# Kernel optimization log

Hardware: AMD Instinct MI355X
Metric: run time of the kernel (lower is better)

## Reference

```python
import jax, jax.numpy as jnp
import numpy as np

B, N, K, C_IN, D = 4, 2048, 16, 480, 64
EPS = 1e-5


def _c1(x, w, b):
    # 1x1 Conv1d: x (B,C,N), w (O,C) -> (B,O,N)
    return jnp.einsum('oc,bcn->bon', w, x) + b[:, None]


def _c2(x, w, b):
    # 1x1 Conv2d: x (B,C,J,N), w (O,C) -> (B,O,J,N)
    return jnp.einsum('oc,bcjn->bojn', w, x) + b[:, None, None]


def _bn(x, g, b):
    # eval-mode BatchNorm2d with running_mean=0, running_var=1
    return x * (g / jnp.sqrt(1.0 + EPS))[:, None, None] + b[:, None, None]


def _mlp_res(x, w1, b1, w2, b2, ws, bs):
    return _c1(jax.nn.relu(_c1(x, w1, b1)), w2, b2) + _c1(x, ws, bs)


def _group(f, idx):
    # f (B,C,N), idx (B,K,N) int -> out[b,c,j,n] = f[b,c,idx[b,j,n]]  -> (B,C,K,N)
    return jax.vmap(lambda ff, ii: ff[:, ii])(f, idx)


def _knn_idx(xyz):
    # xyz (B,3,N) -> idx (B,K,N), excluding the self point (nearest neighbor)
    pts = xyz.transpose(0, 2, 1)  # (B,N,3)
    sq = jnp.sum(pts * pts, -1)
    d2 = sq[:, :, None] + sq[:, None, :] - 2.0 * jnp.einsum('bnd,bmd->bnm', pts, pts)
    _, idx = jax.lax.top_k(-d2, K + 1)  # (B,N,K+1), nearest first
    return idx.transpose(0, 2, 1)[:, 1:, :]  # drop self -> (B,K,N)


def _forward(idx, feature, xyz, bt1_w, bt1_b, bt2_w, bt2_b, bts_w, bts_b,
             q_w, q_b, k_w, k_b, v_w, v_b,
             fd1_w, fd1_b, fd_g, fd_bb, fd2_w, fd2_b,
             fg1_w, fg1_b, fg_g, fg_bb, fg2_w, fg2_b,
             at_w, at_b, m41_w, m41_b, m42_w, m42_b):
    x = _mlp_res(feature, bt1_w, bt1_b, bt2_w, bt2_b, bts_w, bts_b)  # (B,64,N)
    q = _c1(x, q_w, q_b)
    k = _c1(x, k_w, k_b)
    v = _c1(x, v_w, v_b)

    group_xyz = _group(xyz, idx)                       # (B,3,K,N)
    rel_xyz = xyz[:, :, None, :] - group_xyz           # (B,3,K,N)
    pos_enc = _c2(jax.nn.relu(_bn(_c2(rel_xyz, fd1_w, fd1_b), fd_g, fd_bb)), fd2_w, fd2_b)  # (B,64,K,N)

    k_local = _group(k, idx)                           # (B,64,K,N)
    v_local = _group(v, idx)
    qk_rel = q[:, :, None, :] - k_local
    attn = _c2(jax.nn.relu(_bn(_c2(qk_rel + pos_enc, fg1_w, fg1_b), fg_g, fg_bb)), fg2_w, fg2_b)  # (B,64,K,N)

    attn1 = attn.transpose(0, 1, 3, 2)                 # (B,64,N,K)
    # ConvTranspose2d(64,64,(4,1),(4,1)) with kernel==stride: out[b,o,4n+r,f] = sum_c x[b,c,n,f]*W[c,o,r] + bias[o]
    y = jnp.einsum('bcnf,cor->bonrf', attn1, at_w)
    y = y.reshape(y.shape[0], y.shape[1], -1, y.shape[4]) + at_b[None, :, None, None]  # (B,64,4N,K)
    attn = jax.nn.softmax(y, axis=1)

    value_rel = (v_local + pos_enc).transpose(0, 1, 3, 2)   # (B,64,N,K)
    value = jnp.repeat(value_rel, 4, axis=2)                # nearest upsample (4,1) -> (B,64,4N,K)

    res = jnp.einsum('bmnf,bmnf->bmn', attn, value)         # (B,64,4N)
    identity = jnp.repeat(x, 4, axis=2)                     # nearest upsample x4 -> (B,64,4N)
    res = res + identity
    completion = _c1(jax.nn.relu(_c1(res, m41_w, m41_b)), m42_w, m42_b)  # (B,3,4N)
    return completion, res


def setup_inputs() -> dict:
    key = jax.random.key(0)
    ks = jax.random.split(key, 24)
    i = iter(range(24))

    def w(shape):
        return (jax.random.normal(ks[next(i)], shape, dtype=jnp.float32) * 0.05)

    z = lambda n: jnp.zeros((n,), jnp.float32)
    o = lambda n: jnp.ones((n,), jnp.float32)
    return {
        'feature': jax.random.normal(ks[next(i)], (B, C_IN, N), dtype=jnp.float32),
        'xyz': jax.random.normal(ks[next(i)], (B, 3, N), dtype=jnp.float32),
        'bt1_w': w((D, C_IN)), 'bt1_b': z(D),
        'bt2_w': w((D, D)), 'bt2_b': z(D),
        'bts_w': w((D, C_IN)), 'bts_b': z(D),
        'q_w': w((D, D)), 'q_b': z(D),
        'k_w': w((D, D)), 'k_b': z(D),
        'v_w': w((D, D)), 'v_b': z(D),
        'fd1_w': w((D, 3)), 'fd1_b': z(D), 'fd_g': o(D), 'fd_bb': z(D),
        'fd2_w': w((D, D)), 'fd2_b': z(D),
        'fg1_w': w((4 * D, D)), 'fg1_b': z(4 * D), 'fg_g': o(4 * D), 'fg_bb': z(4 * D),
        'fg2_w': w((D, 4 * D)), 'fg2_b': z(D),
        'at_w': w((D, D, 4)), 'at_b': z(D),
        'm41_w': w((D, D)), 'm41_b': z(D),
        'm42_w': w((3, D)), 'm42_b': z(3),
    }


def reference(feature, xyz, bt1_w, bt1_b, bt2_w, bt2_b, bts_w, bts_b,
              q_w, q_b, k_w, k_b, v_w, v_b,
              fd1_w, fd1_b, fd_g, fd_bb, fd2_w, fd2_b,
              fg1_w, fg1_b, fg_g, fg_bb, fg2_w, fg2_b,
              at_w, at_b, m41_w, m41_b, m42_w, m42_b):
    idx = _knn_idx(xyz)
    return _forward(idx, feature, xyz, bt1_w, bt1_b, bt2_w, bt2_b, bts_w, bts_b,
                    q_w, q_b, k_w, k_b, v_w, v_b,
                    fd1_w, fd1_b, fd_g, fd_bb, fd2_w, fd2_b,
                    fg1_w, fg1_b, fg_g, fg_bb, fg2_w, fg2_b,
                    at_w, at_b, m41_w, m41_b, m42_w, m42_b)
```

## Files before the change

kernel.cpp:

```cpp
#include <hip/hip_runtime.h>

#define B_ 4
#define N_ 2048
#define K_ 16
#define CIN_ 480
#define UPN_ 8192
#define M_ (B_*N_*K_)
#define MX_ (B_*N_)
#define KCAP 448

#define KNN_BLK 2048
#define TR_BLK  1920
#define PREP_BLK 1047

typedef unsigned int u32;
typedef unsigned short u16;
typedef unsigned long long u64;
typedef __attribute__((ext_vector_type(8))) short short8;
typedef __attribute__((ext_vector_type(4))) float f32x4;

#define DEV static __device__ __forceinline__

DEV float b2f(u16 h){ return __uint_as_float(((u32)h)<<16); }
DEV u16 f2b(float f){
  u32 u = __float_as_uint(f);
  u32 r = u + 0x7fffu + ((u>>16)&1u);
  return (u16)(r>>16);
}
DEV u32 cvtpk(float a, float b){
  u32 r; asm("v_cvt_pk_bf16_f32 %0, %1, %2" : "=v"(r) : "v"(a), "v"(b));
  return r;
}
DEV u64 cvtpk4(float a, float b, float c, float d){
  return (u64)cvtpk(a,b) | ((u64)cvtpk(c,d)<<32);
}
DEV bool detect_bf(const void* fg){ return ((((const u32*)fg)[0]) & 0xFFFFu) == 0x3F80u; }
DEV float ld(const void* p, int i, bool bf){
  return bf ? b2f(((const u16*)p)[i]) : ((const float*)p)[i];
}
DEV u64 makekey(float d2, int m){
  u32 bits = __float_as_uint(d2);
  bits = (bits & 0x80000000u) ? ~bits : (bits | 0x80000000u);
  return ((u64)bits<<32) | (u32)m;
}
DEV int swz64 (int row, int colByte){ return row*128 + (colByte ^ ((row&7)<<4)); }
DEV int swz128(int row, int colByte){ return row*256 + (colByte ^ ((row&7)<<4)); }

__global__ __launch_bounds__(256) void setup_kernel(
    const void* __restrict__ feature, const void* __restrict__ xyz,
    const void* __restrict__ bt1_w, const void* __restrict__ bt1_b,
    const void* __restrict__ bt2_w, const void* __restrict__ bt2_b,
    const void* __restrict__ bts_w, const void* __restrict__ bts_b,
    const void* __restrict__ q_w, const void* __restrict__ q_b,
    const void* __restrict__ k_w, const void* __restrict__ k_b,
    const void* __restrict__ v_w, const void* __restrict__ v_b,
    const void* __restrict__ fd1_w, const void* __restrict__ fd1_b,
    const void* __restrict__ fd_g, const void* __restrict__ fd_bb,
    const void* __restrict__ fd2_w, const void* __restrict__ fd2_b,
    const void* __restrict__ fg1_w, const void* __restrict__ fg1_b,
    const void* __restrict__ fg_g, const void* __restrict__ fg_bb,
    const void* __restrict__ fg2_w, const void* __restrict__ fg2_b,
    const void* __restrict__ at_w, const void* __restrict__ at_b,
    const void* __restrict__ m41_w, const void* __restrict__ m41_b,
    const void* __restrict__ m42_w, const void* __restrict__ m42_b,
    float* __restrict__ W, u16* __restrict__ WB,
    u16* __restrict__ fxbT, float* __restrict__ fxyz, int* __restrict__ idx)
{
  __shared__ alignas(16) unsigned char smem[50208];
  int blkid = blockIdx.x;
  bool bf = detect_bf(fd_g);

  if(blkid < KNN_BLK){
    float* px = (float*)smem;
    float* py = px + N_;
    float* pz = py + N_;
    float* sq = pz + N_;
    u64*  sbuf = (u64*)(sq + N_);
    u64*  smin = sbuf + 4*KCAP;
    int*  scnt = (int*)(smin + 256);
    u64*  stau = (u64*)(scnt + 256);
    int bx = blkid & 511;
    int b = blkid >> 9;
    int base = b*3*N_;
    bool w0 = (bx==0);
    for(int i=threadIdx.x;i<N_;i+=256){
      float xx=ld(xyz,base+i,bf), yy=ld(xyz,base+N_+i,bf), zz=ld(xyz,base+2*N_+i,bf);
      px[i]=xx; py[i]=yy; pz[i]=zz; sq[i]=xx*xx+yy*yy+zz*zz;
      if(w0){ fxyz[base+i]=xx; fxyz[base+N_+i]=yy; fxyz[base+2*N_+i]=zz; }
    }
    __syncthreads();
    int w = threadIdx.x>>6, l = threadIdx.x&63;
    int q = bx*4 + w;
    float qx=px[q], qy=py[q], qz=pz[q], qs=sq[q];
    float d2c[32];
    u64 best=~0ull;
    #pragma unroll
    for(int j=0;j<32;j++){
      int m = l*32 + ((j+l)&31);
      float d2 = (qs+sq[m]) - 2.0f*(qx*px[m]+qy*py[m]+qz*pz[m]);
      d2c[j]=d2;
      u64 key = makekey(d2, m);
      best = key<best ? key : best;
    }
    smin[w*64+l]=best;
    __syncthreads();
    {
      int rank=0;
      for(int i=0;i<64;i++) rank += (smin[w*64+i] < best);
      if(rank==16) stau[w] = best;
    }
    __syncthreads();
    u64 tau = stau[w];
    int myc=0;
    #pragma unroll
    for(int j=0;j<32;j++){
      int m = l*32 + ((j+l)&31);
      myc += (makekey(d2c[j], m) <= tau);
    }
    scnt[w*64+l]=myc;
    __syncthreads();
    int off=0, tot=0;
    for(int i=0;i<64;i++){
      int c = scnt[w*64+i];
      tot += c;
      off += (i<l) ? c : 0;
    }
    #pragma unroll
    for(int j=0;j<32;j++){
      int m = l*32 + ((j+l)&31);
      u64 key = makekey(d2c[j], m);
      if(key<=tau && off<KCAP){ sbuf[w*KCAP+off]=key; off++; }
    }
    __syncthreads();
    if(tot>KCAP) tot=KCAP;
    for(int p=l; p<tot; p+=64){
      u64 kk = sbuf[w*KCAP+p];
      int rk=0;
      for(int i=0;i<tot;i++) rk += (sbuf[w*KCAP+i] < kk);
      if(rk>=1 && rk<17) idx[(b*K_+(rk-1))*N_+q] = ((int)(kk & 0xffffffffu)) & (N_-1);
    }
    return;
  }

  if(blkid < KNN_BLK + TR_BLK){
    u16 (*s)[34] = (u16(*)[34])smem;
    int t = blkid - KNN_BLK;
    int ntile = t & 31;  int rest = t >> 5;
    int ctile = rest % 15; int b = rest / 15;
    int tx = threadIdx.x & 31, ty = threadIdx.x >> 5;
    u64 base = (u64)b*CIN_*N_;
    #pragma unroll
    for(int r=0;r<4;r++){
      int c = ctile*32 + ty + r*8;
      u64 i = base + (u64)c*N_ + ntile*64 + tx*2;
      u32 v;
      if(bf) v = *(const u32*)((const u16*)feature + i);
      else {
        float a0=((const float*)feature)[i], a1=((const float*)feature)[i+1];
        v = (u32)f2b(a0) | ((u32)f2b(a1)<<16);
      }
      s[tx*2  ][ty + r*8] = (u16)v;
      s[tx*2+1][ty + r*8] = (u16)(v>>16);
    }
    __syncthreads();
    #pragma unroll
    for(int r=0;r<4;r++){
      int i2 = r*256 + threadIdx.x;
      int nrow = i2 >> 4, cp = i2 & 15;
      u32 v = *(const u32*)&s[nrow][cp*2];
      int n = ntile*64 + nrow;
      *(u32*)(fxbT + (u64)b*N_*CIN_ + (u64)n*CIN_ + ctile*32 + cp*2) = v;
    }
    return;
  }

  int t = (blkid - (KNN_BLK + TR_BLK))*256 + threadIdx.x;
  const float inv = 0.9999950000374997f;
  if(t < 30720) return; t -= 30720;
  if(t < 30720) return; t -= 30720;
  if(t < 4096) return; t -= 4096;
  if(t < 4096) return; t -= 4096;
  if(t < 4096) return; t -= 4096;
  if(t < 4096) return; t -= 4096;
  if(t < 256){
    int o=t>>2, j=t&3; float s = ld(fd_g,o,bf)*inv;
    W[77824+t] = (j<3) ? s*ld(fd1_w,o*3+j,bf) : (s*ld(fd1_b,o,bf) + ld(fd_bb,o,bf));
    return;
  } t -= 256;
  if(t < 4096) return; t -= 4096;
  if(t < 16384) return; t -= 16384;
  if(t < 256){ float s=ld(fg_g,t,bf)*inv; W[98560+t] = s*ld(fg1_b,t,bf) + ld(fg_bb,t,bf); return; } t -= 256;
  if(t < 16384) return; t -= 16384;
  if(t < 16384) return; t -= 16384;
  if(t < 4096){ int m=t>>6, o=t&63; W[131584+t] = ld(m41_w,o*64+m,bf); return; } t -= 4096;
  if(t < 192){ W[135680+t] = ld(m42_w,t,bf); return; } t -= 192;
  if(t < 64){ W[135872+t] = ld(bt1_b,t,bf); return; } t -= 64;
  if(t < 64){ W[135936+t] = ld(bts_b,t,bf); return; } t -= 64;
  if(t < 64){ W[136000+t] = ld(bt2_b,t,bf); return; } t -= 64;
  if(t < 64){ W[136064+t] = ld(q_b,t,bf); return; } t -= 64;
  if(t < 64){ W[136128+t] = ld(k_b,t,bf); return; } t -= 64;
  if(t < 64){ W[136192+t] = ld(v_b,t,bf); return; } t -= 64;
  if(t < 64){ W[136256+t] = ld(fd2_b,t,bf); return; } t -= 64;
  if(t < 64){ W[136320+t] = ld(fg2_b,t,bf); return; } t -= 64;
  if(t < 64){ W[136384+t] = ld(at_b,t,bf); return; } t -= 64;
  if(t < 64){ W[136448+t] = ld(m41_b,t,bf); return; } t -= 64;
  if(t < 3){ W[136512+t] = ld(m42_b,t,bf); return; } t -= 3;
  if(t < 16384){ int o=t>>6; float s=ld(fg_g,o,bf)*inv; WB[t] = f2b(s*ld(fg1_w,t,bf)); return; } t -= 16384;
  if(t < 16384){ WB[16384+t] = f2b(ld(fg2_w,t,bf)); return; } t -= 16384;
  if(t < 16384){ int j=t>>6, c=t&63;
                 WB[32768+t] = f2b(ld(at_w,(c*64+(j&63))*4+(j>>6),bf)); return; } t -= 16384;
  if(t < 256){ W[136576+t] = ld(at_b,t&63,bf); return; } t -= 256;
  if(t < 4096){ WB[49152+t] = f2b(ld(fd2_w,t,bf)); return; } t -= 4096;
  if(t < 30720){ WB[53248+t] = f2b(ld(bt1_w,t,bf)); return; } t -= 30720;
  if(t < 30720){ WB[83968+t] = f2b(ld(bts_w,t,bf)); return; } t -= 30720;
  if(t < 4096){ WB[114688+t] = f2b(ld(bt2_w,t,bf)); return; } t -= 4096;
  if(t < 4096){ WB[118784+t] = f2b(ld(q_w,t,bf)); return; } t -= 4096;
  if(t < 4096){ WB[122880+t] = f2b(ld(k_w,t,bf)); return; } t -= 4096;
  if(t < 4096){ WB[126976+t] = f2b(ld(v_w,t,bf)); return; }
}

__global__ __launch_bounds__(256) void gemm480_mfma(const u16* __restrict__ A,
    const u16* __restrict__ Wt, const float* __restrict__ bias,
    u16* __restrict__ hout, float* __restrict__ xsout)
{
  int tid=threadIdx.x, w=tid>>6, lane=tid&63;
  int rbase=(blockIdx.x*4+w)*16;
  int cbase=blockIdx.y*64;
  int lr=lane&15, lk=(lane>>4)*8;
  f32x4 acc[4];
  #pragma unroll
  for(int j=0;j<4;j++) acc[j]=(f32x4){0.f,0.f,0.f,0.f};
  for(int kc=0;kc<CIN_;kc+=32){
    short8 a = *(const short8*)(A + (u64)(rbase+lr)*CIN_ + kc + lk);
    #pragma unroll
    for(int tj=0;tj<4;tj++){
      short8 bb = *(const short8*)(Wt + (u64)(cbase+tj*16+lr)*CIN_ + kc + lk);
      acc[tj] = __builtin_amdgcn_mfma_f32_16x16x32_bf16(a, bb, acc[tj], 0,0,0);
    }
  }
  int rq=(lane>>4)*4;
  #pragma unroll
  for(int tj=0;tj<4;tj++){
    int col = cbase + tj*16 + lr;
    float bv = bias[col];
    #pragma unroll
    for(int reg=0;reg<4;reg++){
      u64 row = rbase + rq + reg;
      float vv = acc[tj][reg] + bv;
      if(blockIdx.y==0) hout[row*64 + col] = f2b(fmaxf(vv,0.f));
      else              xsout[row*64 + (col-64)] = vv;
    }
  }
}

__global__ __launch_bounds__(256) void xqkv_mfma(const u16* __restrict__ A,
    const u16* __restrict__ Wbt2, const float* __restrict__ bbt2,
    const float* __restrict__ xs,
    const u16* __restrict__ Wqkv, const float* __restrict__ bqkv,
    float* __restrict__ x, float* __restrict__ qkvout)
{
  __shared__ alignas(16) unsigned char lds[8192];
  int tid=threadIdx.x, w=tid>>6, lane=tid&63;
  int lr=lane&15, lk=(lane>>4)*8, rq=(lane>>4)*4;
  unsigned char* Lw = lds + w*2048;
  u64 rbase=(u64)(blockIdx.x*4+w)*16;

  {
    f32x4 ax[4];
    #pragma unroll
    for(int i=0;i<4;i++) ax[i]=(f32x4){0.f,0.f,0.f,0.f};
    #pragma unroll
    for(int kc=0;kc<64;kc+=32){
      short8 hf = *(const short8*)(A + (rbase+lr)*64 + kc + lk);
      #pragma unroll
      for(int t=0;t<4;t++){
        short8 wf = *(const short8*)(Wbt2 + (u64)(t*16+lr)*64 + kc + lk);
        ax[t] = __builtin_amdgcn_mfma_f32_16x16x32_bf16(wf, hf, ax[t], 0,0,0);
      }
    }
    #pragma unroll
    for(int t=0;t<4;t++){
      f32x4 bb = *(const f32x4*)(bbt2 + t*16 + rq);
      f32x4 sv = *(const f32x4*)(xs + (rbase+lr)*64 + t*16 + rq);
      f32x4 xv;
      #pragma unroll
      for(int reg=0;reg<4;reg++) xv[reg] = ax[t][reg] + bb[reg] + sv[reg];
      *(f32x4*)(x + (rbase+lr)*64 + t*16 + rq) = xv;
      *(u64*)(Lw + swz64(lr, (t*16+rq)*2)) = cvtpk4(xv[0],xv[1],xv[2],xv[3]);
    }
  }
  __syncthreads();
  #pragma unroll
  for(int g=0;g<3;g++){
    f32x4 aq[4];
    #pragma unroll
    for(int i=0;i<4;i++) aq[i]=(f32x4){0.f,0.f,0.f,0.f};
    #pragma unroll
    for(int kc=0;kc<64;kc+=32){
      short8 hf = *(const short8*)(Lw + swz64(lr, (kc+lk)*2));
      #pragma unroll
      for(int t=0;t<4;t++){
        short8 wf = *(const short8*)(Wqkv + (u64)(g*64+t*16+lr)*64 + kc + lk);
        aq[t] = __builtin_amdgcn_mfma_f32_16x16x32_bf16(wf, hf, aq[t], 0,0,0);
      }
    }
    #pragma unroll
    for(int t=0;t<4;t++){
      f32x4 bq = *(const f32x4*)(bqkv + g*64 + t*16 + rq);
      f32x4 ov;
      #pragma unroll
      for(int reg=0;reg<4;reg++) ov[reg] = aq[t][reg] + bq[reg];
      *(f32x4*)(qkvout + (rbase+lr)*192 + g*64 + t*16 + rq) = ov;
    }
  }
}

__global__ __launch_bounds__(256) void fused_chain(
    const int* __restrict__ idx, const float* __restrict__ fxyz,
    const float* __restrict__ qkv, const float* __restrict__ x,
    const float* __restrict__ fd1f,
    const u16* __restrict__ Wfd2, const float* __restrict__ bfd2,
    const u16* __restrict__ Wfg1, const float* __restrict__ bfg1,
    const u16* __restrict__ Wfg2, const float* __restrict__ bfg2,
    const u16* __restrict__ Wat,  const float* __restrict__ bat,
    const float* __restrict__ cm41T, const float* __restrict__ cm41b,
    const float* __restrict__ cm42f, const float* __restrict__ cm42b,
    const void* __restrict__ det, void* __restrict__ out)
{
  __shared__ alignas(16) unsigned char lds[32768];
  int tid = threadIdx.x;
  int w = tid>>6, lane = tid&63;
  int lr = lane&15, lk = (lane>>4)*8, rq = (lane>>4)*4;

  int erow = tid>>2, ecg = tid&3;
  int el = erow>>4, ef = erow&15;
  int bn_e = blockIdx.x*4 + el;
  int b_e = bn_e>>11, n_e = bn_e&(N_-1);
  int jn = idx[(b_e*K_+ef)*N_ + n_e] & (N_-1);

  {
    const float* xb = fxyz + (u64)b_e*3*N_;
    float rx = xb[n_e]      - xb[jn];
    float ry = xb[N_+n_e]   - xb[N_+jn];
    float rz = xb[2*N_+n_e] - xb[2*N_+jn];
    #pragma unroll
    for(int gg=0; gg<4; gg++){
      float tv[4];
      #pragma unroll
      for(int j=0;j<4;j++){
        f32x4 wv = *(const f32x4*)(fd1f + ((ecg*4+gg)*4+j)*4);
        tv[j] = fmaxf(wv[0]*rx + wv[1]*ry + wv[2]*rz + wv[3], 0.f);
      }
      *(u64*)(lds + swz64(erow, (ecg*4+gg)*8)) = cvtpk4(tv[0],tv[1],tv[2],tv[3]);
    }
  }
  __syncthreads();

  {
    f32x4 acc[4];
    #pragma unroll
    for(int i=0;i<4;i++) acc[i]=(f32x4){0.f,0.f,0.f,0.f};
    #pragma unroll
    for(int kc=0;kc<64;kc+=32){
      short8 wf = *(const short8*)(Wfd2 + (u64)(w*16+lr)*64 + kc + lk);
      #pragma unroll
      for(int ti=0;ti<4;ti++){
        short8 tf = *(const short8*)(lds + swz64(ti*16+lr, (kc+lk)*2));
        acc[ti] = __builtin_amdgcn_mfma_f32_16x16x32_bf16(wf, tf, acc[ti], 0,0,0);
      }
    }
    f32x4 b4 = *(const f32x4*)(bfd2 + w*16 + rq);
    #pragma unroll
    for(int ti=0;ti<4;ti++)
      *(u64*)(lds + 8192 + swz64(ti*16+lr, (w*16+rq)*2)) =
        cvtpk4(acc[ti][0]+b4[0], acc[ti][1]+b4[1], acc[ti][2]+b4[2], acc[ti][3]+b4[3]);
  }
  __syncthreads();

  {
    int mg = ecg*16;
    const float* qrow = qkv + (u64)(b_e*N_+n_e)*192 + mg;
    const float* krow = qkv + (u64)(b_e*N_+jn)*192 + 64 + mg;
    const float* vrow = qkv + (u64)(b_e*N_+jn)*192 + 128 + mg;
    #pragma unroll
    for(int g2=0; g2<4; g2++){
      f32x4 qv = *(const f32x4*)(qrow + g2*4);
      f32x4 kv = *(const f32x4*)(krow + g2*4);
      f32x4 vv = *(const f32x4*)(vrow + g2*4);
      int cb = (mg + g2*4)*2;
      u64 pw = *(const u64*)(lds + 8192 + swz64(erow, cb));
      float p0=b2f((u16)pw), p1=b2f((u16)(pw>>16)), p2=b2f((u16)(pw>>32)), p3=b2f((u16)(pw>>48));
      *(u64*)(lds + swz64(erow, cb)) =
        cvtpk4(qv[0]-kv[0]+p0, qv[1]-kv[1]+p1, qv[2]-kv[2]+p2, qv[3]-kv[3]+p3);
      *(u64*)(lds + 8192 + swz64(erow, cb)) =
        cvtpk4(vv[0]+p0, vv[1]+p1, vv[2]+p2, vv[3]+p3);
    }
  }
  __syncthreads();

  float vreg[16];
  #pragma unroll
  for(int f2=0; f2<16; f2++)
    vreg[f2] = b2f(*(const u16*)(lds + 8192 + swz64(w*16+f2, lane*2)));

  f32x4 gacc[4];
  #pragma unroll
  for(int i=0;i<4;i++) gacc[i]=(f32x4){0.f,0.f,0.f,0.f};
  #pragma unroll
  for(int half=0; half<2; half++){
    {
      f32x4 hacc[2][4];
      #pragma unroll
      for(int i=0;i<2;i++)
        #pragma unroll
        for(int j=0;j<4;j++) hacc[i][j]=(f32x4){0.f,0.f,0.f,0.f};
      #pragma unroll
      for(int kc=0;kc<64;kc+=32){
        short8 wf[2], af[4];
        #pragma unroll
        for(int ti=0;ti<2;ti++)
          wf[ti] = *(const short8*)(Wfg1 + (u64)(half*128 + w*32 + ti*16 + lr)*64 + kc + lk);
        #pragma unroll
        for(int tj=0;tj<4;tj++)
          af[tj] = *(const short8*)(lds + swz64(tj*16+lr, (kc+lk)*2));
        #pragma unroll
        for(int ti=0;ti<2;ti++)
          #pragma unroll
          for(int tj=0;tj<4;tj++)
            hacc[ti][tj] = __builtin_amdgcn_mfma_f32_16x16x32_bf16(wf[ti], af[tj], hacc[ti][tj], 0,0,0);
      }
      #pragma unroll
      for(int ti=0;ti<2;ti++){
        f32x4 b4 = *(const f32x4*)(bfg1 + half*128 + w*32 + ti*16 + rq);
        #pragma unroll
        for(int tj=0;tj<4;tj++){
          int row = tj*16 + lr;
          *(u64*)(lds + 16384 + swz128(row, (w*32+ti*16+rq)*2)) =
            cvtpk4(fmaxf(hacc[ti][tj][0]+b4[0],0.f), fmaxf(hacc[ti][tj][1]+b4[1],0.f),
                   fmaxf(hacc[ti][tj][2]+b4[2],0.f), fmaxf(hacc[ti][tj][3]+b4[3],0.f));
        }
      }
    }
    __syncthreads();
    #pragma unroll
    for(int kc=0;kc<128;kc+=32){
      short8 wf = *(const short8*)(Wfg2 + (u64)(w*16+lr)*256 + half*128 + kc + lk);
      #pragma unroll
      for(int tj=0;tj<4;tj++){
        short8 hf = *(const short8*)(lds + 16384 + swz128(tj*16+lr, (kc+lk)*2));
        gacc[tj] = __builtin_amdgcn_mfma_f32_16x16x32_bf16(wf, hf, gacc[tj], 0,0,0);
      }
    }
    __syncthreads();
  }

  {
    f32x4 b4 = *(const f32x4*)(bfg2 + w*16 + rq);
    #pragma unroll
    for(int tj=0;tj<4;tj++)
      *(u64*)(lds + swz64(tj*16+lr, (w*16+rq)*2)) =
        cvtpk4(gacc[tj][0]+b4[0], gacc[tj][1]+b4[1], gacc[tj][2]+b4[2], gacc[tj][3]+b4[3]);
  }
  __syncthreads();

  float aout[4];
  int srow = tid>>2, sub = tid&3;
  #pragma unroll
  for(int r=0;r<4;r++){
    {
      f32x4 acc[4];
      #pragma unroll
      for(int i=0;i<4;i++) acc[i]=(f32x4){0.f,0.f,0.f,0.f};
      #pragma unroll
      for(int kc=0;kc<64;kc+=32){
        short8 wf = *(const short8*)(Wat + (u64)(r*64 + w*16 + lr)*64 + kc + lk);
        #pragma unroll
        for(int tj=0;tj<4;tj++){
          short8 gf = *(const short8*)(lds + swz64(tj*16+lr, (kc+lk)*2));
          acc[tj] = __builtin_amdgcn_mfma_f32_16x16x32_bf16(wf, gf, acc[tj], 0,0,0);
        }
      }
      f32x4 b4 = *(const f32x4*)(bat + r*64 + w*16 + rq);
      #pragma unroll
      for(int tj=0;tj<4;tj++)
        *(u64*)(lds + 16384 + swz64(tj*16+lr, (w*16+rq)*2)) =
          cvtpk4(acc[tj][0]+b4[0], acc[tj][1]+b4[1], acc[tj][2]+b4[2], acc[tj][3]+b4[3]);
    }
    __syncthreads();
    {
      float yv[16];
      uint4 pk0 = *(const uint4*)(lds + 16384 + swz64(srow, sub*32));
      uint4 pk1 = *(const uint4*)(lds + 16384 + swz64(srow, sub*32 + 16));
      yv[0]=__uint_as_float(pk0.x<<16); yv[1]=__uint_as_float(pk0.x&0xffff0000u);
      yv[2]=__uint_as_float(pk0.y<<16); yv[3]=__uint_as_float(pk0.y&0xffff0000u);
      yv[4]=__uint_as_float(pk0.z<<16); yv[5]=__uint_as_float(pk0.z&0xffff0000u);
      yv[6]=__uint_as_float(pk0.w<<16); yv[7]=__uint_as_float(pk0.w&0xffff0000u);
      yv[8]=__uint_as_float(pk1.x<<16); yv[9]=__uint_as_float(pk1.x&0xffff0000u);
      yv[10]=__uint_as_float(pk1.y<<16); yv[11]=__uint_as_float(pk1.y&0xffff0000u);
      yv[12]=__uint_as_float(pk1.z<<16); yv[13]=__uint_as_float(pk1.z&0xffff0000u);
      yv[14]=__uint_as_float(pk1.w<<16); yv[15]=__uint_as_float(pk1.w&0xffff0000u);
      float mx = yv[0];
      #pragma unroll
      for(int m=1;m<16;m++) mx = fmaxf(mx, yv[m]);
      mx = fmaxf(mx, __shfl_xor(mx, 1));
      mx = fmaxf(mx, __shfl_xor(mx, 2));
      float sm = 0.f;
      #pragma unroll
      for(int m=0;m<16;m++){ float e = __expf(yv[m]-mx); yv[m]=e; sm+=e; }
      sm += __shfl_xor(sm, 1);
      sm += __shfl_xor(sm, 2);
      float rinv = 1.0f/sm;
      uint4 o0, o1;
      o0.x = cvtpk(yv[0]*rinv, yv[1]*rinv);  o0.y = cvtpk(yv[2]*rinv, yv[3]*rinv);
      o0.z = cvtpk(yv[4]*rinv, yv[5]*rinv);  o0.w = cvtpk(yv[6]*rinv, yv[7]*rinv);
      o1.x = cvtpk(yv[8]*rinv, yv[9]*rinv);  o1.y = cvtpk(yv[10]*rinv, yv[11]*rinv);
      o1.z = cvtpk(yv[12]*rinv, yv[13]*rinv); o1.w = cvtpk(yv[14]*rinv, yv[15]*rinv);
      *(uint4*)(lds + 8192 + swz64(srow, sub*32))      = o0;
      *(uint4*)(lds + 8192 + swz64(srow, sub*32 + 16)) = o1;
    }
    __syncthreads();
    {
      float a = 0.f;
      #pragma unroll
      for(int f2=0; f2<16; f2++)
        a += b2f(*(const u16*)(lds + 8192 + swz64(w*16+f2, lane*2))) * vreg[f2];
      aout[r] = a;
    }
  }

  int bn = blockIdx.x*4 + w;
  int b = bn>>11, n = bn&(N_-1);
  float xv = x[(u64)bn*64 + lane];
  u64 off = 98304 + ((u64)(b*64+lane))*UPN_ + (u64)n*4;
  bool bf = detect_bf(det);
  float rv0, rv1, rv2, rv3;
  if(bf){
    u64 pk = cvtpk4(aout[0]+xv, aout[1]+xv, aout[2]+xv, aout[3]+xv);
    *(u64*)((u16*)out + off) = pk;
    rv0 = b2f((u16)pk); rv1 = b2f((u16)(pk>>16));
    rv2 = b2f((u16)(pk>>32)); rv3 = b2f((u16)(pk>>48));
  } else {
    f32x4 pk = {aout[0]+xv, aout[1]+xv, aout[2]+xv, aout[3]+xv};
    *(f32x4*)((float*)out + off) = pk;
    rv0 = pk[0]; rv1 = pk[1]; rv2 = pk[2]; rv3 = pk[3];
  }
  float* L = (float*)(lds + w*1024);
  *(f32x4*)(L + lane*4) = (f32x4){rv0, rv1, rv2, rv3};
  f32x4 acc4;
  {
    float bo = cm41b[lane];
    acc4 = (f32x4){bo, bo, bo, bo};
    for(int c=0;c<64;c++){
      float wv = cm41T[c*64 + lane];
      f32x4 rr = *(const f32x4*)(L + c*4);
      acc4[0] += wv*rr[0]; acc4[1] += wv*rr[1];
      acc4[2] += wv*rr[2]; acc4[3] += wv*rr[3];
    }
  }
  f32x4 h2 = {fmaxf(acc4[0],0.f), fmaxf(acc4[1],0.f),
              fmaxf(acc4[2],0.f), fmaxf(acc4[3],0.f)};
  *(f32x4*)(L + lane*4) = h2;
  if(lane < 12){
    int coord = lane>>2, r2 = lane&3;
    float sum = cm42b[coord];
    for(int o=0;o<64;o++)
      sum += cm42f[coord*64+o] * L[o*4 + r2];
    u64 base = (u64)b*3*UPN_ + (u64)coord*UPN_ + (u64)n*4 + r2;
    if(bf) ((u16*)out)[base] = f2b(sum);
    else   ((float*)out)[base] = sum;
  }
}

extern "C" void kernel_launch(void* const* d_in, const int* in_sizes, int n_in,
                              void* d_out, int out_size, void* d_ws, size_t ws_size,
                              hipStream_t stream)
{
  (void)in_sizes; (void)n_in; (void)out_size; (void)ws_size;
  const void* feature=d_in[0];
  const void* xyz   =d_in[1];
  const void* bt1_w =d_in[2];  const void* bt1_b=d_in[3];
  const void* bt2_w =d_in[4];  const void* bt2_b=d_in[5];
  const void* bts_w =d_in[6];  const void* bts_b=d_in[7];
  const void* q_w   =d_in[8];  const void* q_b =d_in[9];
  const void* k_w   =d_in[10]; const void* k_b =d_in[11];
  const void* v_w   =d_in[12]; const void* v_b =d_in[13];
  const void* fd1_w =d_in[14]; const void* fd1_b=d_in[15];
  const void* fd_g  =d_in[16]; const void* fd_bb=d_in[17];
  const void* fd2_w =d_in[18]; const void* fd2_b=d_in[19];
  const void* fg1_w =d_in[20]; const void* fg1_b=d_in[21];
  const void* fg_g  =d_in[22]; const void* fg_bb=d_in[23];
  const void* fg2_w =d_in[24]; const void* fg2_b=d_in[25];
  const void* at_w  =d_in[26]; const void* at_b =d_in[27];
  const void* m41_w =d_in[28]; const void* m41_b=d_in[29];
  const void* m42_w =d_in[30]; const void* m42_b=d_in[31];

  char* ws=(char*)d_ws;
  float* W   =(float*)(ws);
  u16*  WB   =(u16*)  (ws + 589824);
  int*  idx  =(int*)  (ws + 851968);
  float* x   =(float*)(ws + 1376256);
  float* qkv =(float*)(ws + 3473408);
  u16*  h    =(u16*)  (ws + 9764864);
  float* xs  =(float*)(ws + 10813440);
  u16*  fxbT =(u16*)  (ws + 114622464);
  float* fxyz=(float*)(ws + 122486784);

  const float* W_fd1f = W+77824;
  const float* W_fg1fb= W+98560;
  const float* W_m41T = W+131584;
  const float* W_m42  = W+135680;
  const float* Wb_g480= W+135872;
  const float* Wb_bt2 = W+136000;
  const float* Wb_qkv = W+136064;
  const float* Wb_fd2 = W+136256;
  const float* Wb_fg2 = W+136320;
  const float* Wb_m41 = W+136448;
  const float* Wb_m42 = W+136512;
  const float* W_atb256 = W+136576;
  const u16* WB_fg1  = WB;
  const u16* WB_fg2  = WB+16384;
  const u16* WB_at   = WB+32768;
  const u16* WB_fd2  = WB+49152;
  const u16* WB_g480 = WB+53248;
  const u16* WB_bt2  = WB+114688;
  const u16* WB_qkv  = WB+118784;

  setup_kernel<<<KNN_BLK+TR_BLK+PREP_BLK,256,0,stream>>>(feature, xyz,
      bt1_w,bt1_b,bt2_w,bt2_b,bts_w,bts_b,q_w,q_b,k_w,k_b,
      v_w,v_b,fd1_w,fd1_b,fd_g,fd_bb,fd2_w,fd2_b,fg1_w,fg1_b,fg_g,fg_bb,fg2_w,fg2_b,
      at_w,at_b,m41_w,m41_b,m42_w,m42_b,W,WB,fxbT,fxyz,idx);
  gemm480_mfma<<<dim3(MX_/64,2),256,0,stream>>>(fxbT, WB_g480, Wb_g480, h, xs);
  xqkv_mfma<<<MX_/64,256,0,stream>>>(h, WB_bt2, Wb_bt2, xs, WB_qkv, Wb_qkv, x, qkv);
  fused_chain<<<B_*N_/4,256,0,stream>>>(idx, fxyz, qkv, x, W_fd1f,
      WB_fd2, Wb_fd2, WB_fg1, W_fg1fb, WB_fg2, Wb_fg2, WB_at, W_atb256,
      W_m41T, Wb_m41, W_m42, Wb_m42, fd_g, d_out);
}
```

Measured before the change: 252.2 us.

## Split final m41/m42 MLP tail out of fused_chain into separate kernel

Moves the trailing two-layer point MLP (m41 relu then m42 to xyz) out of the fused attention kernel into a new comp_kernel. The new kernel gives each thread one upsampled point and half the output channels, re-reading the stored attention output from global memory. Work is split across lanes and combined with a shuffle. This removes the serialized per-wave tail, where only 12 lanes did the final reduction, and frees LDS and registers in fused_chain. In exchange it adds an extra launch and a global round trip of the 64-channel tensor.

```diff
diff --git a/kernel.cpp b/kernel.cpp
--- a/kernel.cpp
+++ b/kernel.cpp
@@ -323,8 +323,6 @@
     const u16* __restrict__ Wfg1, const float* __restrict__ bfg1,
     const u16* __restrict__ Wfg2, const float* __restrict__ bfg2,
     const u16* __restrict__ Wat,  const float* __restrict__ bat,
-    const float* __restrict__ cm41T, const float* __restrict__ cm41b,
-    const float* __restrict__ cm42f, const float* __restrict__ cm42b,
     const void* __restrict__ det, void* __restrict__ out)
 {
   __shared__ alignas(16) unsigned char lds[32768];
@@ -532,42 +530,65 @@
   int b = bn>>11, n = bn&(N_-1);
   float xv = x[(u64)bn*64 + lane];
   u64 off = 98304 + ((u64)(b*64+lane))*UPN_ + (u64)n*4;
-  bool bf = detect_bf(det);
-  float rv0, rv1, rv2, rv3;
-  if(bf){
-    u64 pk = cvtpk4(aout[0]+xv, aout[1]+xv, aout[2]+xv, aout[3]+xv);
-    *(u64*)((u16*)out + off) = pk;
-    rv0 = b2f((u16)pk); rv1 = b2f((u16)(pk>>16));
-    rv2 = b2f((u16)(pk>>32)); rv3 = b2f((u16)(pk>>48));
+  if(detect_bf(det)){
+    *(u64*)((u16*)out + off) = cvtpk4(aout[0]+xv, aout[1]+xv, aout[2]+xv, aout[3]+xv);
   } else {
     f32x4 pk = {aout[0]+xv, aout[1]+xv, aout[2]+xv, aout[3]+xv};
     *(f32x4*)((float*)out + off) = pk;
-    rv0 = pk[0]; rv1 = pk[1]; rv2 = pk[2]; rv3 = pk[3];
-  }
-  float* L = (float*)(lds + w*1024);
-  *(f32x4*)(L + lane*4) = (f32x4){rv0, rv1, rv2, rv3};
-  f32x4 acc4;
-  {
-    float bo = cm41b[lane];
-    acc4 = (f32x4){bo, bo, bo, bo};
+  }
+}
+
+__global__ __launch_bounds__(128) void comp_kernel(
+  const float* __restrict__ m41T, const float* __restrict__ m41b,
+  const float* __restrict__ m42f, const float* __restrict__ m42b,
+  const void* __restrict__ det, void* __restrict__ out)
+{
+  int tid = threadIdx.x;
+  int wv = tid>>6, lane = tid&63;
+  int half = lane>>5, l32 = lane&31;
+  int g = blockIdx.x*64 + wv*32 + l32;
+  int un = g & (UPN_-1);
+  int b = g >> 13;
+  bool bf = detect_bf(det);
+  float acc[32];
+  #pragma unroll
+  for(int o=0;o<32;o++) acc[o] = m41b[half*32+o];
+  if(bf){
+    const u16* rr = (const u16*)out + 98304 + (u64)b*64*UPN_ + un;
     for(int c=0;c<64;c++){
-      float wv = cm41T[c*64 + lane];
-      f32x4 rr = *(const f32x4*)(L + c*4);
-      acc4[0] += wv*rr[0]; acc4[1] += wv*rr[1];
-      acc4[2] += wv*rr[2]; acc4[3] += wv*rr[3];
-    }
-  }
-  f32x4 h2 = {fmaxf(acc4[0],0.f), fmaxf(acc4[1],0.f),
-              fmaxf(acc4[2],0.f), fmaxf(acc4[3],0.f)};
-  *(f32x4*)(L + lane*4) = h2;
-  if(lane < 12){
-    int coord = lane>>2, r2 = lane&3;
-    float sum = cm42b[coord];
-    for(int o=0;o<64;o++)
-      sum += cm42f[coord*64+o] * L[o*4 + r2];
-    u64 base = (u64)b*3*UPN_ + (u64)coord*UPN_ + (u64)n*4 + r2;
-    if(bf) ((u16*)out)[base] = f2b(sum);
-    else   ((float*)out)[base] = sum;
+      float rv = b2f(rr[(u64)c*UPN_]);
+      const float* w = m41T + c*64 + half*32;
+      #pragma unroll
+      for(int o=0;o<32;o++) acc[o] += w[o]*rv;
+    }
+  } else {
+    const float* rr = (const float*)out + 98304 + (u64)b*64*UPN_ + un;
+    for(int c=0;c<64;c++){
+      float rv = rr[(u64)c*UPN_];
+      const float* w = m41T + c*64 + half*32;
+      #pragma unroll
+      for(int o=0;o<32;o++) acc[o] += w[o]*rv;
+    }
+  }
+  float c0=0.f, c1=0.f, c2=0.f;
+  #pragma unroll
+  for(int o=0;o<32;o++){
+    float hv = fmaxf(acc[o],0.f);
+    c0 += m42f[half*32+o]*hv; c1 += m42f[64+half*32+o]*hv; c2 += m42f[128+half*32+o]*hv;
+  }
+  c0 += __shfl_xor(c0, 32);
+  c1 += __shfl_xor(c1, 32);
+  c2 += __shfl_xor(c2, 32);
+  if(half==0){
+    c0 += m42b[0]; c1 += m42b[1]; c2 += m42b[2];
+    u64 base = (u64)b*3*UPN_ + un;
+    if(bf){
+      u16* cp = (u16*)out;
+      cp[base]=f2b(c0); cp[base+UPN_]=f2b(c1); cp[base+2*UPN_]=f2b(c2);
+    } else {
+      float* cp = (float*)out;
+      cp[base]=c0; cp[base+UPN_]=c1; cp[base+2*UPN_]=c2;
+    }
   }
 }
 
@@ -632,6 +653,6 @@
   gemm480_mfma<<<dim3(MX_/64,2),256,0,stream>>>(fxbT, WB_g480, Wb_g480, h, xs);
   xqkv_mfma<<<MX_/64,256,0,stream>>>(h, WB_bt2, Wb_bt2, xs, WB_qkv, Wb_qkv, x, qkv);
   fused_chain<<<B_*N_/4,256,0,stream>>>(idx, fxyz, qkv, x, W_fd1f,
-      WB_fd2, Wb_fd2, WB_fg1, W_fg1fb, WB_fg2, Wb_fg2, WB_at, W_atb256,
-      W_m41T, Wb_m41, W_m42, Wb_m42, fd_g, d_out);
-}
+      WB_fd2, Wb_fd2, WB_fg1, W_fg1fb, WB_fg2, Wb_fg2, WB_at, W_atb256, fd_g, d_out);
+  comp_kernel<<<512,128,0,stream>>>(W_m41T, Wb_m41, W_m42, Wb_m42, fd_g, d_out);
+}
```

After: 264.2 us. 4.8% more time.
